# Optimization experiments

Measured on AMD Instinct MI355X. Metric: run time of the kernel, lower is better.

The kernel has to match this reference:

```python
import jax, jax.numpy as jnp
import numpy as np

N_NODES = 100000
N_EDGES = 1600000
NODE_DIM = 16
EDGE_DIM = 16
OUT_DIM = 16
H = 64  # edge/node/global hidden size
N_GRAPHS = 1


def _glorot(key, shape):
    fan_in, fan_out = shape[0], shape[1]
    lim = np.sqrt(6.0 / (fan_in + fan_out))
    return jax.random.uniform(key, shape, jnp.float32, -lim, lim)


def setup_inputs() -> dict:
    key = jax.random.key(0)
    ks = jax.random.split(key, 16)
    x = jax.random.normal(ks[0], (N_NODES, NODE_DIM), jnp.float32)
    edge_attr = jax.random.normal(ks[1], (N_EDGES, EDGE_DIM), jnp.float32)
    u = jax.random.normal(ks[2], (N_GRAPHS, H), jnp.float32)
    senders = jax.random.randint(ks[3], (N_EDGES,), 0, N_NODES, jnp.int32)
    receivers = jax.random.randint(ks[4], (N_EDGES,), 0, N_NODES, jnp.int32)
    node_gidx = jnp.zeros((N_NODES,), jnp.int32)
    edge_gidx = jnp.zeros((N_EDGES,), jnp.int32)
    # EdgeBlock MLP: in = edge + 2*node + global_h
    W_eb = _glorot(ks[5], (EDGE_DIM + 2 * NODE_DIM + H, H)); b_eb = jnp.zeros((H,), jnp.float32)
    # NodeBlock MLP: in = node + edge_h + global_h
    W_nb = _glorot(ks[6], (NODE_DIM + H + H, H)); b_nb = jnp.zeros((H,), jnp.float32)
    # GlobalBlock MLP: in = node_h + edge_h + global_h
    W_gb = _glorot(ks[7], (H + H + H, H)); b_gb = jnp.zeros((H,), jnp.float32)
    # node decoder: in = 2*edge_h + node_h + global_h -> H -> out
    W_d1 = _glorot(ks[8], (2 * H + H + H, H)); b_d1 = jnp.zeros((H,), jnp.float32)
    W_d2 = _glorot(ks[9], (H, OUT_DIM)); b_d2 = jnp.zeros((OUT_DIM,), jnp.float32)
    return dict(x=x, edge_attr=edge_attr, u=u, senders=senders, receivers=receivers,
                node_gidx=node_gidx, edge_gidx=edge_gidx,
                W_eb=W_eb, b_eb=b_eb, W_nb=W_nb, b_nb=b_nb, W_gb=W_gb, b_gb=b_gb,
                W_d1=W_d1, b_d1=b_d1, W_d2=W_d2, b_d2=b_d2)


def _segment_mean(data, ids, num_segments):
    s = jax.ops.segment_sum(data, ids, num_segments=num_segments)
    cnt = jax.ops.segment_sum(jnp.ones((data.shape[0], 1), data.dtype), ids, num_segments=num_segments)
    return s / jnp.maximum(cnt, 1.0)


def reference(x, edge_attr, u, senders, receivers, node_gidx, edge_gidx,
              W_eb, b_eb, W_nb, b_nb, W_gb, b_gb, W_d1, b_d1, W_d2, b_d2):
    # ---- GN1: EdgeBlock (gather -> concat -> linear+relu) ----
    e_in = jnp.concatenate([edge_attr, x[receivers], x[senders], u[edge_gidx]], axis=-1)  # [E, 112]
    e_h = jax.nn.relu(e_in @ W_eb + b_eb)  # [E, H]
    # ---- GN1: NodeBlock (scatter_add of received edges) ----
    agg_recv = jax.ops.segment_sum(e_h, receivers, num_segments=x.shape[0])  # [N, H]
    n_in = jnp.concatenate([agg_recv, x, u[node_gidx]], axis=-1)
    n_h = jax.nn.relu(n_in @ W_nb + b_nb)  # [N, H]
    # ---- GN1: GlobalBlock (scatter_mean reductions) ----
    e_mean = _segment_mean(e_h, edge_gidx, u.shape[0])  # [B, H]
    n_mean = _segment_mean(n_h, node_gidx, u.shape[0])  # [B, H]
    g_in = jnp.concatenate([e_mean, n_mean, u], axis=-1)
    u2 = jax.nn.relu(g_in @ W_gb + b_gb)  # [B, H]
    # ---- GN2: node decoder block (scatter_mean sent + received edges) ----
    agg_recv2 = _segment_mean(e_h, receivers, x.shape[0])
    agg_sent2 = _segment_mean(e_h, senders, x.shape[0])
    d_in = jnp.concatenate([agg_recv2, agg_sent2, n_h, u2[node_gidx]], axis=-1)  # [N, 256]
    out = jax.nn.relu(d_in @ W_d1 + b_d1) @ W_d2 + b_d2  # [N, out_dim]
    return out
```

## Files before the change

### kernel.cpp

```cpp
#include <hip/hip_runtime.h>


typedef unsigned int uint;
typedef unsigned short ushort;
typedef __attribute__((ext_vector_type(8))) short bf16x8;
typedef __attribute__((ext_vector_type(4))) float f32x4;

#define BW 128
#define BSHIFT 7
#define NBMAX 784
#define DC 4096
#define EMASK 0x1FFFFFu
#define OMASK 0x1FFFFu

#define LDF4(p) (*reinterpret_cast<const float4*>(p))

__device__ __forceinline__ ushort f2bf(float f) {
  uint u = __float_as_uint(f);
  u += 0x7FFFu + ((u >> 16) & 1u);
  return (ushort)(u >> 16);
}

__device__ __forceinline__ int aswz(int row, int kb) {
  return row * 64 + ((kb ^ (row & 7)) << 3);
}
__device__ __forceinline__ int nswz(int row, int kb) {
  return row * 128 + (((kb & 8) | ((kb ^ row) & 7)) << 3);
}
__device__ __forceinline__ int aswz192(int row, int kb) {
  return row * 192 + (((kb & 24) | ((kb ^ row) & 7)) << 3);
}

__global__ __launch_bounds__(256) void init_kernel(
    const float* __restrict__ x, ushort* __restrict__ xb, int n16, int nxb,
    const int* __restrict__ receivers, const int* __restrict__ senders,
    uint* __restrict__ bcnt_r, uint* __restrict__ bcnt_s, int E, int NB,
    const float* __restrict__ u, const float* __restrict__ W_eb,
    const float* __restrict__ b_eb, const float* __restrict__ W_nb,
    const float* __restrict__ b_nb, const float* __restrict__ W_d1,
    const float* __restrict__ W_d2, float* __restrict__ eb_init,
    float* __restrict__ nb_init, ushort* __restrict__ wt_lin,
    ushort* __restrict__ wnb_img, ushort* __restrict__ wtd1_img,
    ushort* __restrict__ w2_img) {
  if (blockIdx.x == 0) {
    int j = threadIdx.x;
    if (j >= 64) return;
    float ae = b_eb[j], an = b_nb[j];
    for (int k = 0; k < 64; ++k) {
      float uk = u[k];
      ae = fmaf(uk, W_eb[(48 + k) * 64 + j], ae);
      an = fmaf(uk, W_nb[(80 + k) * 64 + j], an);
    }
    eb_init[j] = ae;
    nb_init[j] = an;
    for (int k = 0; k < 64; ++k)
      wt_lin[j * 64 + k] = (k < 48) ? f2bf(W_eb[k * 64 + j]) : (ushort)0;
    for (int k = 0; k < 128; ++k) {
      ushort v = (k < 80) ? f2bf(W_nb[k * 64 + j]) : (ushort)0;
      wnb_img[nswz(j, k >> 3) + (k & 7)] = v;
    }
    for (int k = 0; k < 192; ++k)
      wtd1_img[aswz192(j, k >> 3) + (k & 7)] = f2bf(W_d1[k * 64 + j]);
    if (j < 16)
      for (int k = 0; k < 64; ++k)
        w2_img[aswz(j, k >> 3) + (k & 7)] = f2bf(W_d2[k * 16 + j]);
    return;
  }
  if (blockIdx.x <= nxb) {
    int i = (blockIdx.x - 1) * 256 + threadIdx.x;
    if (i * 4 >= n16) return;
    float4 a = LDF4(x + i * 4);
    ushort4 o = {f2bf(a.x), f2bf(a.y), f2bf(a.z), f2bf(a.w)};
    *reinterpret_cast<ushort4*>(xb + i * 4) = o;
    return;
  }
  __shared__ uint hr[NBMAX], hs[NBMAX];
  int t = threadIdx.x;
  int bid = blockIdx.x - 1 - nxb;
  for (int i = t; i < NB; i += 256) { hr[i] = 0; hs[i] = 0; }
  __syncthreads();
  int stride = 64 * 256;
  for (int e = bid * 256 + t; e < E; e += stride) {
    atomicAdd(&hr[receivers[e] >> BSHIFT], 1u);
    atomicAdd(&hs[senders[e] >> BSHIFT], 1u);
  }
  __syncthreads();
  for (int i = t; i < NB; i += 256) {
    if (hr[i]) atomicAdd(&bcnt_r[i], hr[i]);
    if (hs[i]) atomicAdd(&bcnt_s[i], hs[i]);
  }
}

__global__ __launch_bounds__(256) void bscan_kernel(
    const uint* __restrict__ bcnt_r, const uint* __restrict__ bcnt_s,
    uint* __restrict__ start_r, uint* __restrict__ start_s,
    uint* __restrict__ cur_r, uint* __restrict__ cur_s, int E, int NB) {
  __shared__ uint ts[256];
  int t = threadIdx.x;
  #pragma unroll
  for (int pass = 0; pass < 2; ++pass) {
    const uint* cnt = pass ? bcnt_s : bcnt_r;
    uint* start = pass ? start_s : start_r;
    uint* cur = pass ? cur_s : cur_r;
    uint loc[4]; uint tsum = 0;
    #pragma unroll
    for (int q = 0; q < 4; ++q) {
      int i = t * 4 + q;
      loc[q] = (i < NB) ? cnt[i] : 0;
      tsum += loc[q];
    }
    ts[t] = tsum;
    __syncthreads();
    for (int off = 1; off < 256; off <<= 1) {
      uint a = (t >= off) ? ts[t - off] : 0;
      __syncthreads();
      ts[t] += a;
      __syncthreads();
    }
    uint run = ts[t] - tsum;
    #pragma unroll
    for (int q = 0; q < 4; ++q) {
      int i = t * 4 + q;
      if (i < NB) { start[i] = run; cur[i] = run; run += loc[q]; }
    }
    if (t == 0) start[NB] = (uint)E;
    __syncthreads();
  }
}

__global__ __launch_bounds__(256) void distribute_kernel(
    const int* __restrict__ receivers, const int* __restrict__ senders,
    uint* __restrict__ gcur_r, uint* __restrict__ gcur_s,
    uint2* __restrict__ tmp_r, uint2* __restrict__ tmp_s, int E, int NB) {
  __shared__ uint hist[NBMAX], lstart[NBMAX], cur[NBMAX], gbase[NBMAX];
  __shared__ uint2 ids[DC];
  __shared__ ushort idsB[DC];
  __shared__ uint ts[256];
  int dir = blockIdx.x & 1;
  const int* key = dir ? senders : receivers;
  const int* oth = dir ? receivers : senders;
  uint* g_cursor = dir ? gcur_s : gcur_r;
  uint2* tmp = dir ? tmp_s : tmp_r;
  int t = threadIdx.x;
  int base = (blockIdx.x >> 1) * DC;
  int cact = min(DC, E - base);
  for (int i = t; i < NB; i += 256) hist[i] = 0;
  __syncthreads();
  for (int k = 0; k < DC / 256; ++k) {
    int j = k * 256 + t;
    if (j < cact) atomicAdd(&hist[key[base + j] >> BSHIFT], 1u);
  }
  __syncthreads();
  {
    uint loc[4]; uint tsum = 0;
    #pragma unroll
    for (int q = 0; q < 4; ++q) {
      int i = t * 4 + q;
      loc[q] = (i < NB) ? hist[i] : 0;
      tsum += loc[q];
    }
    ts[t] = tsum;
    __syncthreads();
    for (int off = 1; off < 256; off <<= 1) {
      uint a = (t >= off) ? ts[t - off] : 0;
      __syncthreads();
      ts[t] += a;
      __syncthreads();
    }
    uint run = ts[t] - tsum;
    #pragma unroll
    for (int q = 0; q < 4; ++q) {
      int i = t * 4 + q;
      if (i < NB) { lstart[i] = run; cur[i] = run; run += loc[q]; }
    }
  }
  __syncthreads();
  for (int i = t; i < NB; i += 256)
    if (hist[i]) gbase[i] = atomicAdd(&g_cursor[i], hist[i]);
  for (int k = 0; k < DC / 256; ++k) {
    int j = k * 256 + t;
    if (j < cact) {
      int e = base + j;
      int kk = key[e];
      uint b = (uint)(kk >> BSHIFT);
      uint slot = atomicAdd(&cur[b], 1u);
      ids[slot] = uint2{((uint)(kk & (BW - 1)) << 21) | (uint)e,
                        (uint)oth[e]};
      idsB[slot] = (ushort)b;
    }
  }
  __syncthreads();
  for (int j = t; j < cact; j += 256) {
    uint b2 = idsB[j];
    tmp[gbase[b2] + ((uint)j - lstart[b2])] = ids[j];
  }
}

__global__ __launch_bounds__(256) void bucketsort_kernel(
    const uint2* __restrict__ tmp_r, const uint2* __restrict__ tmp_s,
    const uint* __restrict__ start_r, const uint* __restrict__ start_s,
    uint2* __restrict__ srt_r, uint2* __restrict__ srt_s,
    uint* __restrict__ cnt_r, uint* __restrict__ cnt_s, int N) {
  __shared__ uint hist[BW], pfx[BW], cur[BW];
  int d = blockIdx.x & 1;
  int b = blockIdx.x >> 1;
  const uint2* tmp = d ? tmp_s : tmp_r;
  const uint* start = d ? start_s : start_r;
  uint2* srt = d ? srt_s : srt_r;
  uint* cnt = d ? cnt_s : cnt_r;
  int t = threadIdx.x;
  if (t < BW) hist[t] = 0;
  __syncthreads();
  int beg = (int)start[b], end = (int)start[b + 1];
  for (int i = beg + t; i < end; i += 256)
    atomicAdd(&hist[tmp[i].x >> 21], 1u);
  __syncthreads();
  if (t < BW) pfx[t] = hist[t];
  __syncthreads();
  for (int off = 1; off < BW; off <<= 1) {
    uint a = 0;
    if (t < BW && t >= off) a = pfx[t - off];
    __syncthreads();
    if (t < BW) pfx[t] += a;
    __syncthreads();
  }
  if (t < BW) cur[t] = pfx[t] - hist[t];
  __syncthreads();
  uint bhi = (uint)b << 17;
  for (int i = beg + t; i < end; i += 256) {
    uint2 v = tmp[i];
    uint nl = v.x >> 21;
    uint p = beg + atomicAdd(&cur[nl], 1u);
    srt[p] = uint2{v.x, bhi | v.y};
  }
  int nbase = b * BW;
  if (t < BW && nbase + t < N) cnt[nbase + t] = hist[t];
}

__global__ __launch_bounds__(256, 4) void escatter_kernel(
    const float* __restrict__ edge_attr, const ushort* __restrict__ xb,
    const uint2* __restrict__ srt_r, const uint2* __restrict__ srt_s,
    const ushort* __restrict__ wt_lin, const float* __restrict__ eb_init,
    float* __restrict__ sum_recv, float* __restrict__ sum_sent, int E,
    int ntiles) {
  __shared__ float Clds[4][16 * 72];
  __shared__ int nodeW[4][16];
  int t = threadIdx.x;
  int wid = t >> 6, l = t & 63;
  int lrow = l & 15, lk = l >> 4;
  bf16x8 b0[4], b1[4];
  float ebi[4];
  #pragma unroll
  for (int nt = 0; nt < 4; ++nt) {
    const ushort* wr = wt_lin + (nt * 16 + lrow) * 64;
    b0[nt] = *reinterpret_cast<const bf16x8*>(wr + lk * 8);
    b1[nt] = *reinterpret_cast<const bf16x8*>(wr + 32 + lk * 8);
    ebi[nt] = eb_init[nt * 16 + lrow];
  }
  const bf16x8 zero8 = {0, 0, 0, 0, 0, 0, 0, 0};
  int dir = blockIdx.x & 1;
  const uint2* srt = dir ? srt_s : srt_r;
  float* sum = dir ? sum_sent : sum_recv;
  int gw = (blockIdx.x >> 1) * 4 + wid;
  int nw = (gridDim.x >> 1) * 4;

  uint2 vC = {0, 0}, vN = {0, 0};
  bf16x8 a0C = zero8, a1C = zero8;

  if (gw < ntiles) {
    vC = srt[min(gw * 16 + lrow, E - 1)];
    int e = (int)(vC.x & EMASK);
    int kn = (int)((vC.y >> 17) * BW + (vC.x >> 21));
    int on = (int)(vC.y & OMASK);
    int s = dir ? kn : on;
    int r = dir ? on : kn;
    if (lk < 2) {
      const float* ap = edge_attr + (size_t)e * 16 + lk * 8;
      float4 f0 = LDF4(ap), f1 = LDF4(ap + 4);
      union { ushort h[8]; bf16x8 v; } pk;
      pk.h[0] = f2bf(f0.x); pk.h[1] = f2bf(f0.y);
      pk.h[2] = f2bf(f0.z); pk.h[3] = f2bf(f0.w);
      pk.h[4] = f2bf(f1.x); pk.h[5] = f2bf(f1.y);
      pk.h[6] = f2bf(f1.z); pk.h[7] = f2bf(f1.w);
      a0C = pk.v;
      a1C = *reinterpret_cast<const bf16x8*>(xb + (size_t)s * 16 + lk * 8);
    } else {
      a0C = *reinterpret_cast<const bf16x8*>(xb + (size_t)r * 16 +
                                             (lk - 2) * 8);
      a1C = zero8;
    }
  }
  if (gw + nw < ntiles) vN = srt[min((gw + nw) * 16 + lrow, E - 1)];

  for (int tile = gw; tile < ntiles; tile += nw) {
    bool hasN = (tile + nw) < ntiles;
    bool has2 = (tile + 2 * nw) < ntiles;
    bf16x8 a0N = zero8, a1N = zero8;
    if (hasN) {
      int e = (int)(vN.x & EMASK);
      int kn = (int)((vN.y >> 17) * BW + (vN.x >> 21));
      int on = (int)(vN.y & OMASK);
      int s = dir ? kn : on;
      int r = dir ? on : kn;
      if (lk < 2) {
        const float* ap = edge_attr + (size_t)e * 16 + lk * 8;
        float4 f0 = LDF4(ap), f1 = LDF4(ap + 4);
        union { ushort h[8]; bf16x8 v; } pk;
        pk.h[0] = f2bf(f0.x); pk.h[1] = f2bf(f0.y);
        pk.h[2] = f2bf(f0.z); pk.h[3] = f2bf(f0.w);
        pk.h[4] = f2bf(f1.x); pk.h[5] = f2bf(f1.y);
        pk.h[6] = f2bf(f1.z); pk.h[7] = f2bf(f1.w);
        a0N = pk.v;
        a1N = *reinterpret_cast<const bf16x8*>(xb + (size_t)s * 16 + lk * 8);
      } else {
        a0N = *reinterpret_cast<const bf16x8*>(xb + (size_t)r * 16 +
                                               (lk - 2) * 8);
      }
    }
    uint2 v2 = {0, 0};
    if (has2) v2 = srt[min((tile + 2 * nw) * 16 + lrow, E - 1)];
    if (lk == 0)
      nodeW[wid][lrow] = (int)((vC.y >> 17) * BW + (vC.x >> 21));
    f32x4 acc[4];
    #pragma unroll
    for (int nt = 0; nt < 4; ++nt) {
      acc[nt] = f32x4{ebi[nt], ebi[nt], ebi[nt], ebi[nt]};
      acc[nt] =
          __builtin_amdgcn_mfma_f32_16x16x32_bf16(a0C, b0[nt], acc[nt], 0, 0, 0);
      acc[nt] =
          __builtin_amdgcn_mfma_f32_16x16x32_bf16(a1C, b1[nt], acc[nt], 0, 0, 0);
    }
    int m0 = (l >> 4) * 4;
    #pragma unroll
    for (int nt = 0; nt < 4; ++nt) {
      #pragma unroll
      for (int reg = 0; reg < 4; ++reg) {
        Clds[wid][(m0 + reg) * 72 + nt * 16 + lrow] =
            fmaxf(acc[nt][reg], 0.f);
      }
    }
    int vc = min(16, E - tile * 16);
    float accum = 0.f;
    int prev = nodeW[wid][0];
    for (int mm = 0; mm < vc; ++mm) {
      int nd = nodeW[wid][mm];
      float v = Clds[wid][mm * 72 + l];
      if (nd != prev) {
        atomicAdd(&sum[(size_t)prev * 64 + l], accum);
        accum = 0.f;
        prev = nd;
      }
      accum += v;
    }
    atomicAdd(&sum[(size_t)prev * 64 + l], accum);
    vC = vN; a0C = a0N; a1C = a1N; vN = v2;
  }
}

__global__ __launch_bounds__(256, 2) void node_mfma_kernel(
    const float* __restrict__ sum_recv, const ushort* __restrict__ xb,
    const ushort* __restrict__ wnb_img, const float* __restrict__ nb_init,
    ushort* __restrict__ n_h, float* __restrict__ e_sum,
    float* __restrict__ n_sum, int N) {
  __shared__ ushort Alds[64 * 128];
  __shared__ ushort Wlds[64 * 128];
  __shared__ ushort Clds[4][16 * 72];
  int t = threadIdx.x;
  int base = blockIdx.x * 64;
  {
    const uint4* src = reinterpret_cast<const uint4*>(wnb_img);
    uint4* dst = reinterpret_cast<uint4*>(Wlds);
    #pragma unroll
    for (int i = 0; i < 4; ++i) dst[t + 256 * i] = src[t + 256 * i];
  }
  {
    int m = t >> 2, part = t & 3;
    int n = base + m;
    bool val = n < N;
    if (part < 2) {
      #pragma unroll
      for (int q = 0; q < 4; ++q) {
        int c = part * 4 + q;
        union { ushort h[8]; uint4 qq; } pk;
        if (val) {
          const float* src = sum_recv + (size_t)n * 64 + c * 8;
          float4 f0 = LDF4(src), f1 = LDF4(src + 4);
          pk.h[0] = f2bf(f0.x); pk.h[1] = f2bf(f0.y);
          pk.h[2] = f2bf(f0.z); pk.h[3] = f2bf(f0.w);
          pk.h[4] = f2bf(f1.x); pk.h[5] = f2bf(f1.y);
          pk.h[6] = f2bf(f1.z); pk.h[7] = f2bf(f1.w);
        } else {
          pk.qq = uint4{0, 0, 0, 0};
        }
        *reinterpret_cast<uint4*>(&Alds[nswz(m, c)]) = pk.qq;
      }
    } else if (part == 2) {
      uint4 w0 = {0, 0, 0, 0}, w1 = {0, 0, 0, 0};
      if (val) {
        const uint4* xp = reinterpret_cast<const uint4*>(xb + (size_t)n * 16);
        w0 = xp[0]; w1 = xp[1];
      }
      *reinterpret_cast<uint4*>(&Alds[nswz(m, 8)]) = w0;
      *reinterpret_cast<uint4*>(&Alds[nswz(m, 9)]) = w1;
      *reinterpret_cast<uint4*>(&Alds[nswz(m, 10)]) = uint4{0, 0, 0, 0};
      *reinterpret_cast<uint4*>(&Alds[nswz(m, 11)]) = uint4{0, 0, 0, 0};
    } else {
      #pragma unroll
      for (int q = 0; q < 4; ++q)
        *reinterpret_cast<uint4*>(&Alds[nswz(m, 12 + q)]) = uint4{0, 0, 0, 0};
    }
  }
  __syncthreads();
  int wid = t >> 6, l = t & 63;
  int lrow = l & 15, lk = l >> 4;
  int arow = wid * 16 + lrow;
  bf16x8 afr[4];
  #pragma unroll
  for (int g = 0; g < 4; ++g)
    afr[g] = *reinterpret_cast<const bf16x8*>(&Alds[nswz(arow, g * 4 + lk)]);
  f32x4 acc[4];
  #pragma unroll
  for (int nt = 0; nt < 4; ++nt) {
    float nbi = nb_init[nt * 16 + lrow];
    acc[nt] = f32x4{nbi, nbi, nbi, nbi};
    #pragma unroll
    for (int g = 0; g < 4; ++g) {
      bf16x8 b = *reinterpret_cast<const bf16x8*>(
          &Wlds[nswz(nt * 16 + lrow, g * 4 + lk)]);
      acc[nt] =
          __builtin_amdgcn_mfma_f32_16x16x32_bf16(afr[g], b, acc[nt], 0, 0, 0);
    }
  }
  int m0 = (l >> 4) * 4;
  #pragma unroll
  for (int nt = 0; nt < 4; ++nt) {
    #pragma unroll
    for (int reg = 0; reg < 4; ++reg) {
      Clds[wid][(m0 + reg) * 72 + nt * 16 + lrow] =
          f2bf(fmaxf(acc[nt][reg], 0.f));
    }
  }
  __syncthreads();
  int sm = l >> 2, ch = l & 3;
  int gn = base + wid * 16 + sm;
  uint4 c0 = *reinterpret_cast<const uint4*>(&Clds[wid][sm * 72 + ch * 16]);
  uint4 c1 = *reinterpret_cast<const uint4*>(&Clds[wid][sm * 72 + ch * 16 + 8]);
  if (gn < N) {
    uint4* dst = reinterpret_cast<uint4*>(n_h + (size_t)gn * 64 + ch * 16);
    dst[0] = c0;
    dst[1] = c1;
  }
  float* scr = reinterpret_cast<float*>(Alds);
  {
    int col = t & 63, rg = t >> 6;
    float pe = 0.f, pn = 0.f;
    #pragma unroll
    for (int rr = 0; rr < 16; ++rr) {
      int n = base + rg * 16 + rr;
      if (n < N) {
        pe += sum_recv[(size_t)n * 64 + col];
        pn += __uint_as_float((uint)Clds[rg][rr * 72 + col] << 16);
      }
    }
    scr[rg * 64 + col] = pe;
    scr[256 + rg * 64 + col] = pn;
  }
  __syncthreads();
  if (t < 64) {
    float se = scr[t] + scr[64 + t] + scr[128 + t] + scr[192 + t];
    float sn = scr[256 + t] + scr[320 + t] + scr[384 + t] + scr[448 + t];
    atomicAdd(&e_sum[t], se);
    atomicAdd(&n_sum[t], sn);
  }
}

__global__ __launch_bounds__(256, 2) void decoder_mfma_kernel(
    const float* __restrict__ sum_recv, const float* __restrict__ sum_sent,
    const uint* __restrict__ cnt_r, const uint* __restrict__ cnt_s,
    const ushort* __restrict__ n_h, const ushort* __restrict__ wtd1_img,
    const ushort* __restrict__ w2_img, const float* __restrict__ b_d2,
    const float* __restrict__ u, const float* __restrict__ e_sum,
    const float* __restrict__ n_sum, const float* __restrict__ W_gb,
    const float* __restrict__ b_gb, const float* __restrict__ W_d1,
    const float* __restrict__ b_d1, float* __restrict__ out, float invE,
    float invN, int N) {
  __shared__ ushort Alds[64 * 192];
  __shared__ ushort Wlds[64 * 192];
  __shared__ ushort Hlds[64 * 64];
  __shared__ ushort W2lds[16 * 64];
  __shared__ float gin[192], u2s[64], d1i[64];
  int t = threadIdx.x;
  int base = blockIdx.x * 64;
  {
    const uint4* src = reinterpret_cast<const uint4*>(wtd1_img);
    uint4* dst = reinterpret_cast<uint4*>(Wlds);
    #pragma unroll
    for (int i = 0; i < 6; ++i) dst[t + 256 * i] = src[t + 256 * i];
    if (t < 128)
      reinterpret_cast<uint4*>(W2lds)[t] =
          reinterpret_cast<const uint4*>(w2_img)[t];
  }
  {
    int m = t >> 2;
    int n = base + m;
    bool val = n < N;
    float invr = 0.f, invs = 0.f;
    if (val) {
      invr = 1.f / fmaxf((float)cnt_r[n], 1.f);
      invs = 1.f / fmaxf((float)cnt_s[n], 1.f);
    }
    int c0 = (t & 3) * 6;
    for (int c = c0; c < c0 + 6; ++c) {
      union { ushort h[8]; uint4 q; } pk;
      if (val) {
        if (c >= 16) {
          pk.q = *reinterpret_cast<const uint4*>(n_h + (size_t)n * 64 +
                                                 (c - 16) * 8);
        } else {
          const float* src;
          float scl;
          if (c < 8) { src = sum_recv + (size_t)n * 64 + c * 8; scl = invr; }
          else       { src = sum_sent + (size_t)n * 64 + (c - 8) * 8; scl = invs; }
          float4 f0 = LDF4(src), f1 = LDF4(src + 4);
          pk.h[0] = f2bf(f0.x * scl); pk.h[1] = f2bf(f0.y * scl);
          pk.h[2] = f2bf(f0.z * scl); pk.h[3] = f2bf(f0.w * scl);
          pk.h[4] = f2bf(f1.x * scl); pk.h[5] = f2bf(f1.y * scl);
          pk.h[6] = f2bf(f1.z * scl); pk.h[7] = f2bf(f1.w * scl);
        }
      } else {
        pk.q = uint4{0, 0, 0, 0};
      }
      *reinterpret_cast<uint4*>(&Alds[aswz192(m, c)]) = pk.q;
    }
  }
  if (t < 64) {
    gin[t] = e_sum[t] * invE;
    gin[64 + t] = n_sum[t] * invN;
    gin[128 + t] = u[t];
  }
  __syncthreads();
  if (t < 64) {
    float a = b_gb[t];
    for (int k = 0; k < 192; ++k) a = fmaf(gin[k], W_gb[k * 64 + t], a);
    u2s[t] = fmaxf(a, 0.f);
  }
  __syncthreads();
  if (t < 64) {
    float d = b_d1[t];
    for (int k = 0; k < 64; ++k) d = fmaf(u2s[k], W_d1[(192 + k) * 64 + t], d);
    d1i[t] = d;
  }
  __syncthreads();
  int wid = t >> 6, l = t & 63;
  int lrow = l & 15, lk = l >> 4;
  int arow = wid * 16 + lrow;
  bf16x8 afr[6];
  #pragma unroll
  for (int g = 0; g < 6; ++g)
    afr[g] = *reinterpret_cast<const bf16x8*>(&Alds[aswz192(arow, g * 4 + lk)]);
  f32x4 acc[4];
  #pragma unroll
  for (int nt = 0; nt < 4; ++nt) {
    float di = d1i[nt * 16 + lrow];
    acc[nt] = f32x4{di, di, di, di};
    #pragma unroll
    for (int g = 0; g < 6; ++g) {
      bf16x8 b = *reinterpret_cast<const bf16x8*>(
          &Wlds[aswz192(nt * 16 + lrow, g * 4 + lk)]);
      acc[nt] =
          __builtin_amdgcn_mfma_f32_16x16x32_bf16(afr[g], b, acc[nt], 0, 0, 0);
    }
  }
  int m0 = (l >> 4) * 4;
  #pragma unroll
  for (int nt = 0; nt < 4; ++nt) {
    #pragma unroll
    for (int reg = 0; reg < 4; ++reg) {
      int hm = wid * 16 + m0 + reg;
      int hn = nt * 16 + lrow;
      Hlds[hm * 64 + (((hn >> 3) ^ (hm & 7)) << 3) + (hn & 7)] =
          f2bf(fmaxf(acc[nt][reg], 0.f));
    }
  }
  __syncthreads();
  bf16x8 a20 = *reinterpret_cast<const bf16x8*>(&Hlds[aswz(arow, lk)]);
  bf16x8 a21 = *reinterpret_cast<const bf16x8*>(&Hlds[aswz(arow, 4 + lk)]);
  bf16x8 b20 = *reinterpret_cast<const bf16x8*>(&W2lds[aswz(lrow, lk)]);
  bf16x8 b21 = *reinterpret_cast<const bf16x8*>(&W2lds[aswz(lrow, 4 + lk)]);
  float bi = b_d2[lrow];
  f32x4 o = f32x4{bi, bi, bi, bi};
  o = __builtin_amdgcn_mfma_f32_16x16x32_bf16(a20, b20, o, 0, 0, 0);
  o = __builtin_amdgcn_mfma_f32_16x16x32_bf16(a21, b21, o, 0, 0, 0);
  #pragma unroll
  for (int reg = 0; reg < 4; ++reg) {
    int ge = base + wid * 16 + m0 + reg;
    if (ge < N) out[(size_t)ge * 16 + lrow] = o[reg];
  }
}

extern "C" void kernel_launch(void* const* d_in, const int* in_sizes, int n_in,
                              void* d_out, int out_size, void* d_ws,
                              size_t ws_size, hipStream_t stream) {
  const float* x         = (const float*)d_in[0];
  const float* edge_attr = (const float*)d_in[1];
  const float* u         = (const float*)d_in[2];
  const int*   senders   = (const int*)d_in[3];
  const int*   receivers = (const int*)d_in[4];
  const float* W_eb = (const float*)d_in[7];
  const float* b_eb = (const float*)d_in[8];
  const float* W_nb = (const float*)d_in[9];
  const float* b_nb = (const float*)d_in[10];
  const float* W_gb = (const float*)d_in[11];
  const float* b_gb = (const float*)d_in[12];
  const float* W_d1 = (const float*)d_in[13];
  const float* b_d1 = (const float*)d_in[14];
  const float* W_d2 = (const float*)d_in[15];
  const float* b_d2 = (const float*)d_in[16];

  int N = in_sizes[0] / 16;
  int E = in_sizes[1] / 16;
  int NB = (N + BW - 1) >> BSHIFT;
  int NDB = (E + DC - 1) / DC;
  int ntiles = (E + 15) / 16;
  int nxb = (N * 16 / 4 + 255) / 256;

  char* w = (char*)d_ws;
  float* sum_recv = (float*)w;       w += (size_t)N * 64 * 4;
  float* sum_sent = (float*)w;       w += (size_t)N * 64 * 4;
  ushort* n_h = (ushort*)w;          w += (size_t)N * 64 * 2;
  uint2* tmp_r = (uint2*)w;          w += (size_t)E * 8;
  uint2* tmp_s = (uint2*)w;          w += (size_t)E * 8;
  uint2* srt_r = (uint2*)w;          w += (size_t)E * 8;
  uint2* srt_s = (uint2*)w;          w += (size_t)E * 8;
  uint* cnt_r = (uint*)w;            w += (size_t)N * 4;
  uint* cnt_s = (uint*)w;            w += (size_t)N * 4;
  ushort* xb = (ushort*)w;           w += (size_t)N * 16 * 2;
  ushort* wt_lin = (ushort*)w;       w += (size_t)64 * 64 * 2;
  ushort* wnb_img = (ushort*)w;      w += (size_t)64 * 128 * 2;
  ushort* wtd1_img = (ushort*)w;     w += (size_t)64 * 192 * 2;
  ushort* w2_img = (ushort*)w;       w += (size_t)16 * 64 * 2;
  uint* start_r = (uint*)w;          w += (size_t)(NB + 1) * 4;
  uint* start_s = (uint*)w;          w += (size_t)(NB + 1) * 4;
  uint* cur_r = (uint*)w;            w += (size_t)NB * 4;
  uint* cur_s = (uint*)w;            w += (size_t)NB * 4;
  uint* bcnt_r = (uint*)w;           w += (size_t)NBMAX * 4;
  uint* bcnt_s = (uint*)w;           w += (size_t)NBMAX * 4;
  float* e_sum = (float*)w;          w += 64 * 4;
  float* n_sum = (float*)w;          w += 64 * 4;
  float* eb_init = (float*)w;        w += 64 * 4;
  float* nb_init = (float*)w;        w += 64 * 4;

  size_t zero_bytes = (size_t)(2 * NBMAX + 128) * 4;
  hipMemsetAsync(bcnt_r, 0, zero_bytes, stream);
  hipMemsetAsync(sum_recv, 0, (size_t)N * 128 * 4, stream);

  hipLaunchKernelGGL(init_kernel, dim3(1 + nxb + 64), dim3(256), 0, stream, x,
                     xb, N * 16, nxb, receivers, senders, bcnt_r, bcnt_s, E,
                     NB, u, W_eb, b_eb, W_nb, b_nb, W_d1, W_d2, eb_init,
                     nb_init, wt_lin, wnb_img, wtd1_img, w2_img);
  hipLaunchKernelGGL(bscan_kernel, dim3(1), dim3(256), 0, stream, bcnt_r,
                     bcnt_s, start_r, start_s, cur_r, cur_s, E, NB);
  hipLaunchKernelGGL(distribute_kernel, dim3(2 * NDB), dim3(256), 0, stream,
                     receivers, senders, cur_r, cur_s, tmp_r, tmp_s, E, NB);
  hipLaunchKernelGGL(bucketsort_kernel, dim3(2 * NB), dim3(256), 0, stream,
                     tmp_r, tmp_s, start_r, start_s, srt_r, srt_s, cnt_r,
                     cnt_s, N);
  hipLaunchKernelGGL(escatter_kernel, dim3(4096), dim3(256), 0, stream,
                     edge_attr, xb, srt_r, srt_s, wt_lin, eb_init, sum_recv,
                     sum_sent, E, ntiles);
  hipLaunchKernelGGL(node_mfma_kernel, dim3((N + 63) / 64), dim3(256), 0,
                     stream, sum_recv, xb, wnb_img, nb_init, n_h, e_sum,
                     n_sum, N);
  hipLaunchKernelGGL(decoder_mfma_kernel, dim3((N + 63) / 64), dim3(256), 0,
                     stream, sum_recv, sum_sent, cnt_r, cnt_s, n_h, wtd1_img,
                     w2_img, b_d2, u, e_sum, n_sum, W_gb, b_gb, W_d1, b_d1,
                     (float*)d_out, 1.0f / (float)E, 1.0f / (float)N, N);
}
```

Before: 396.2 us.

## Fuse per-bucket local sort into edge MLP scatter kernel

Removes the separate bucketsort kernel and its sorted global arrays. Each escatter block now takes one coarse bucket, stages its entries in LDS in chunks, builds a local node-ordered permutation, and runs the MFMA edge MLP and segmented atomic scatter directly from it. Per-node counts are accumulated atomically into a zeroed buffer. This saves one launch and a full read/write pass over the edge index arrays. In exchange, grid size is tied to the bucket count, it uses more LDS per block, and large buckets go through a serial chunk loop with extra barriers.

```diff
diff --git a/kernel.cpp b/kernel.cpp
--- a/kernel.cpp
+++ b/kernel.cpp
@@ -10,8 +10,8 @@
 #define BSHIFT 7
 #define NBMAX 784
 #define DC 4096
+#define CAP 1536
 #define EMASK 0x1FFFFFu
-#define OMASK 0x1FFFFu
 
 #define LDF4(p) (*reinterpret_cast<const float4*>(p))
 
@@ -196,53 +196,16 @@
   }
 }
 
-__global__ __launch_bounds__(256) void bucketsort_kernel(
+__global__ __launch_bounds__(256, 4) void escatter_kernel(
+    const float* __restrict__ edge_attr, const ushort* __restrict__ xb,
     const uint2* __restrict__ tmp_r, const uint2* __restrict__ tmp_s,
     const uint* __restrict__ start_r, const uint* __restrict__ start_s,
-    uint2* __restrict__ srt_r, uint2* __restrict__ srt_s,
-    uint* __restrict__ cnt_r, uint* __restrict__ cnt_s, int N) {
+    const ushort* __restrict__ wt_lin, const float* __restrict__ eb_init,
+    float* __restrict__ sum_recv, float* __restrict__ sum_sent,
+    uint* __restrict__ cnt_r, uint* __restrict__ cnt_s, int E, int N) {
+  __shared__ uint2 stage[CAP];
+  __shared__ ushort ord[CAP];
   __shared__ uint hist[BW], pfx[BW], cur[BW];
-  int d = blockIdx.x & 1;
-  int b = blockIdx.x >> 1;
-  const uint2* tmp = d ? tmp_s : tmp_r;
-  const uint* start = d ? start_s : start_r;
-  uint2* srt = d ? srt_s : srt_r;
-  uint* cnt = d ? cnt_s : cnt_r;
-  int t = threadIdx.x;
-  if (t < BW) hist[t] = 0;
-  __syncthreads();
-  int beg = (int)start[b], end = (int)start[b + 1];
-  for (int i = beg + t; i < end; i += 256)
-    atomicAdd(&hist[tmp[i].x >> 21], 1u);
-  __syncthreads();
-  if (t < BW) pfx[t] = hist[t];
-  __syncthreads();
-  for (int off = 1; off < BW; off <<= 1) {
-    uint a = 0;
-    if (t < BW && t >= off) a = pfx[t - off];
-    __syncthreads();
-    if (t < BW) pfx[t] += a;
-    __syncthreads();
-  }
-  if (t < BW) cur[t] = pfx[t] - hist[t];
-  __syncthreads();
-  uint bhi = (uint)b << 17;
-  for (int i = beg + t; i < end; i += 256) {
-    uint2 v = tmp[i];
-    uint nl = v.x >> 21;
-    uint p = beg + atomicAdd(&cur[nl], 1u);
-    srt[p] = uint2{v.x, bhi | v.y};
-  }
-  int nbase = b * BW;
-  if (t < BW && nbase + t < N) cnt[nbase + t] = hist[t];
-}
-
-__global__ __launch_bounds__(256, 4) void escatter_kernel(
-    const float* __restrict__ edge_attr, const ushort* __restrict__ xb,
-    const uint2* __restrict__ srt_r, const uint2* __restrict__ srt_s,
-    const ushort* __restrict__ wt_lin, const float* __restrict__ eb_init,
-    float* __restrict__ sum_recv, float* __restrict__ sum_sent, int E,
-    int ntiles) {
   __shared__ float Clds[4][16 * 72];
   __shared__ int nodeW[4][16];
   int t = threadIdx.x;
@@ -259,47 +222,51 @@
   }
   const bf16x8 zero8 = {0, 0, 0, 0, 0, 0, 0, 0};
   int dir = blockIdx.x & 1;
-  const uint2* srt = dir ? srt_s : srt_r;
+  int b = blockIdx.x >> 1;
+  const uint2* tmp = dir ? tmp_s : tmp_r;
+  const uint* start = dir ? start_s : start_r;
   float* sum = dir ? sum_sent : sum_recv;
-  int gw = (blockIdx.x >> 1) * 4 + wid;
-  int nw = (gridDim.x >> 1) * 4;
-
-  uint2 vC = {0, 0}, vN = {0, 0};
-  bf16x8 a0C = zero8, a1C = zero8;
-
-  if (gw < ntiles) {
-    vC = srt[min(gw * 16 + lrow, E - 1)];
-    int e = (int)(vC.x & EMASK);
-    int kn = (int)((vC.y >> 17) * BW + (vC.x >> 21));
-    int on = (int)(vC.y & OMASK);
-    int s = dir ? kn : on;
-    int r = dir ? on : kn;
-    if (lk < 2) {
-      const float* ap = edge_attr + (size_t)e * 16 + lk * 8;
-      float4 f0 = LDF4(ap), f1 = LDF4(ap + 4);
-      union { ushort h[8]; bf16x8 v; } pk;
-      pk.h[0] = f2bf(f0.x); pk.h[1] = f2bf(f0.y);
-      pk.h[2] = f2bf(f0.z); pk.h[3] = f2bf(f0.w);
-      pk.h[4] = f2bf(f1.x); pk.h[5] = f2bf(f1.y);
-      pk.h[6] = f2bf(f1.z); pk.h[7] = f2bf(f1.w);
-      a0C = pk.v;
-      a1C = *reinterpret_cast<const bf16x8*>(xb + (size_t)s * 16 + lk * 8);
-    } else {
-      a0C = *reinterpret_cast<const bf16x8*>(xb + (size_t)r * 16 +
-                                             (lk - 2) * 8);
-      a1C = zero8;
-    }
-  }
-  if (gw + nw < ntiles) vN = srt[min((gw + nw) * 16 + lrow, E - 1)];
-
-  for (int tile = gw; tile < ntiles; tile += nw) {
-    bool hasN = (tile + nw) < ntiles;
-    bool has2 = (tile + 2 * nw) < ntiles;
-    bf16x8 a0N = zero8, a1N = zero8;
-    if (hasN) {
-      int e = (int)(vN.x & EMASK);
-      int kn = (int)((vN.y >> 17) * BW + (vN.x >> 21));
-      int on = (int)(vN.y & OMASK);
+  uint* cnt = dir ? cnt_s : cnt_r;
+  int beg = (int)start[b], end = (int)start[b + 1];
+  int nbase = b * BW;
+
+  for (int cbeg = beg; cbeg < end; cbeg += CAP) {
+    int cc = min(CAP, end - cbeg);
+    if (t < BW) hist[t] = 0;
+    __syncthreads();
+    for (int i = t; i < cc; i += 256) {
+      uint2 v = tmp[cbeg + i];
+      stage[i] = v;
+      atomicAdd(&hist[v.x >> 21], 1u);
+    }
+    __syncthreads();
+    if (t < BW && hist[t] && nbase + t < N) atomicAdd(&cnt[nbase + t], hist[t]);
+    if (t < BW) pfx[t] = hist[t];
+    __syncthreads();
+    for (int off = 1; off < BW; off <<= 1) {
+      uint a = 0;
+      if (t < BW && t >= off) a = pfx[t - off];
+      __syncthreads();
+      if (t < BW) pfx[t] += a;
+      __syncthreads();
+    }
+    if (t < BW) cur[t] = pfx[t] - hist[t];
+    __syncthreads();
+    for (int i = t; i < cc; i += 256) {
+      uint nl = stage[i].x >> 21;
+      uint p = atomicAdd(&cur[nl], 1u);
+      ord[p] = (ushort)i;
+    }
+    __syncthreads();
+    int ntile = (cc + 15) >> 4;
+    uint2 vC = {0, 0}, vN = {0, 0};
+    bf16x8 a0C = zero8, a1C = zero8;
+    if (wid < ntile) {
+      int j = min(wid * 16 + lrow, cc - 1);
+      vC = stage[ord[j]];
+      int e = (int)(vC.x & EMASK);
+      int kn = nbase + (int)(vC.x >> 21);
+      int on = (int)vC.y;
       int s = dir ? kn : on;
       int r = dir ? on : kn;
       if (lk < 2) {
@@ -310,50 +277,75 @@
         pk.h[2] = f2bf(f0.z); pk.h[3] = f2bf(f0.w);
         pk.h[4] = f2bf(f1.x); pk.h[5] = f2bf(f1.y);
         pk.h[6] = f2bf(f1.z); pk.h[7] = f2bf(f1.w);
-        a0N = pk.v;
-        a1N = *reinterpret_cast<const bf16x8*>(xb + (size_t)s * 16 + lk * 8);
+        a0C = pk.v;
+        a1C = *reinterpret_cast<const bf16x8*>(xb + (size_t)s * 16 + lk * 8);
       } else {
-        a0N = *reinterpret_cast<const bf16x8*>(xb + (size_t)r * 16 +
+        a0C = *reinterpret_cast<const bf16x8*>(xb + (size_t)r * 16 +
                                                (lk - 2) * 8);
       }
     }
-    uint2 v2 = {0, 0};
-    if (has2) v2 = srt[min((tile + 2 * nw) * 16 + lrow, E - 1)];
-    if (lk == 0)
-      nodeW[wid][lrow] = (int)((vC.y >> 17) * BW + (vC.x >> 21));
-    f32x4 acc[4];
-    #pragma unroll
-    for (int nt = 0; nt < 4; ++nt) {
-      acc[nt] = f32x4{ebi[nt], ebi[nt], ebi[nt], ebi[nt]};
-      acc[nt] =
-          __builtin_amdgcn_mfma_f32_16x16x32_bf16(a0C, b0[nt], acc[nt], 0, 0, 0);
-      acc[nt] =
-          __builtin_amdgcn_mfma_f32_16x16x32_bf16(a1C, b1[nt], acc[nt], 0, 0, 0);
-    }
-    int m0 = (l >> 4) * 4;
-    #pragma unroll
-    for (int nt = 0; nt < 4; ++nt) {
+    for (int wt = wid; wt < ntile; wt += 4) {
+      int wtN = wt + 4;
+      bf16x8 a0N = zero8, a1N = zero8;
+      if (wtN < ntile) {
+        int j = min(wtN * 16 + lrow, cc - 1);
+        vN = stage[ord[j]];
+        int e = (int)(vN.x & EMASK);
+        int kn = nbase + (int)(vN.x >> 21);
+        int on = (int)vN.y;
+        int s = dir ? kn : on;
+        int r = dir ? on : kn;
+        if (lk < 2) {
+          const float* ap = edge_attr + (size_t)e * 16 + lk * 8;
+          float4 f0 = LDF4(ap), f1 = LDF4(ap + 4);
+          union { ushort h[8]; bf16x8 v; } pk;
+          pk.h[0] = f2bf(f0.x); pk.h[1] = f2bf(f0.y);
+          pk.h[2] = f2bf(f0.z); pk.h[3] = f2bf(f0.w);
+          pk.h[4] = f2bf(f1.x); pk.h[5] = f2bf(f1.y);
+          pk.h[6] = f2bf(f1.z); pk.h[7] = f2bf(f1.w);
+          a0N = pk.v;
+          a1N = *reinterpret_cast<const bf16x8*>(xb + (size_t)s * 16 + lk * 8);
+        } else {
+          a0N = *reinterpret_cast<const bf16x8*>(xb + (size_t)r * 16 +
+                                                 (lk - 2) * 8);
+        }
+      }
+      if (lk == 0) nodeW[wid][lrow] = nbase + (int)(vC.x >> 21);
+      f32x4 acc[4];
       #pragma unroll
-      for (int reg = 0; reg < 4; ++reg) {
-        Clds[wid][(m0 + reg) * 72 + nt * 16 + lrow] =
-            fmaxf(acc[nt][reg], 0.f);
-      }
-    }
-    int vc = min(16, E - tile * 16);
-    float accum = 0.f;
-    int prev = nodeW[wid][0];
-    for (int mm = 0; mm < vc; ++mm) {
-      int nd = nodeW[wid][mm];
-      float v = Clds[wid][mm * 72 + l];
-      if (nd != prev) {
-        atomicAdd(&sum[(size_t)prev * 64 + l], accum);
-        accum = 0.f;
-        prev = nd;
-      }
-      accum += v;
-    }
-    atomicAdd(&sum[(size_t)prev * 64 + l], accum);
-    vC = vN; a0C = a0N; a1C = a1N; vN = v2;
+      for (int nt = 0; nt < 4; ++nt) {
+        acc[nt] = f32x4{ebi[nt], ebi[nt], ebi[nt], ebi[nt]};
+        acc[nt] = __builtin_amdgcn_mfma_f32_16x16x32_bf16(a0C, b0[nt], acc[nt],
+                                                          0, 0, 0);
+        acc[nt] = __builtin_amdgcn_mfma_f32_16x16x32_bf16(a1C, b1[nt], acc[nt],
+                                                          0, 0, 0);
+      }
+      int m0 = (l >> 4) * 4;
+      #pragma unroll
+      for (int nt = 0; nt < 4; ++nt) {
+        #pragma unroll
+        for (int reg = 0; reg < 4; ++reg) {
+          Clds[wid][(m0 + reg) * 72 + nt * 16 + lrow] =
+              fmaxf(acc[nt][reg], 0.f);
+        }
+      }
+      int vc = min(16, cc - wt * 16);
+      float accum = 0.f;
+      int prev = nodeW[wid][0];
+      for (int mm = 0; mm < vc; ++mm) {
+        int nd = nodeW[wid][mm];
+        float v = Clds[wid][mm * 72 + l];
+        if (nd != prev) {
+          atomicAdd(&sum[(size_t)prev * 64 + l], accum);
+          accum = 0.f;
+          prev = nd;
+        }
+        accum += v;
+      }
+      atomicAdd(&sum[(size_t)prev * 64 + l], accum);
+      vC = vN; a0C = a0N; a1C = a1N;
+    }
+    __syncthreads();
   }
 }
 
@@ -621,7 +613,6 @@
   int E = in_sizes[1] / 16;
   int NB = (N + BW - 1) >> BSHIFT;
   int NDB = (E + DC - 1) / DC;
-  int ntiles = (E + 15) / 16;
   int nxb = (N * 16 / 4 + 255) / 256;
 
   char* w = (char*)d_ws;
@@ -630,10 +621,6 @@
   ushort* n_h = (ushort*)w;          w += (size_t)N * 64 * 2;
   uint2* tmp_r = (uint2*)w;          w += (size_t)E * 8;
   uint2* tmp_s = (uint2*)w;          w += (size_t)E * 8;
-  uint2* srt_r = (uint2*)w;          w += (size_t)E * 8;
-  uint2* srt_s = (uint2*)w;          w += (size_t)E * 8;
-  uint* cnt_r = (uint*)w;            w += (size_t)N * 4;
-  uint* cnt_s = (uint*)w;            w += (size_t)N * 4;
   ushort* xb = (ushort*)w;           w += (size_t)N * 16 * 2;
   ushort* wt_lin = (ushort*)w;       w += (size_t)64 * 64 * 2;
   ushort* wnb_img = (ushort*)w;      w += (size_t)64 * 128 * 2;
@@ -643,6 +630,8 @@
   uint* start_s = (uint*)w;          w += (size_t)(NB + 1) * 4;
   uint* cur_r = (uint*)w;            w += (size_t)NB * 4;
   uint* cur_s = (uint*)w;            w += (size_t)NB * 4;
+  uint* cnt_r = (uint*)w;            w += (size_t)N * 4;
+  uint* cnt_s = (uint*)w;            w += (size_t)N * 4;
   uint* bcnt_r = (uint*)w;           w += (size_t)NBMAX * 4;
   uint* bcnt_s = (uint*)w;           w += (size_t)NBMAX * 4;
   float* e_sum = (float*)w;          w += 64 * 4;
@@ -650,8 +639,8 @@
   float* eb_init = (float*)w;        w += 64 * 4;
   float* nb_init = (float*)w;        w += 64 * 4;
 
-  size_t zero_bytes = (size_t)(2 * NBMAX + 128) * 4;
-  hipMemsetAsync(bcnt_r, 0, zero_bytes, stream);
+  size_t zero_bytes = ((size_t)2 * N + 2 * NBMAX + 128) * 4;
+  hipMemsetAsync(cnt_r, 0, zero_bytes, stream);
   hipMemsetAsync(sum_recv, 0, (size_t)N * 128 * 4, stream);
 
   hipLaunchKernelGGL(init_kernel, dim3(1 + nxb + 64), dim3(256), 0, stream, x,
@@ -662,12 +651,9 @@
                      bcnt_s, start_r, start_s, cur_r, cur_s, E, NB);
   hipLaunchKernelGGL(distribute_kernel, dim3(2 * NDB), dim3(256), 0, stream,
                      receivers, senders, cur_r, cur_s, tmp_r, tmp_s, E, NB);
-  hipLaunchKernelGGL(bucketsort_kernel, dim3(2 * NB), dim3(256), 0, stream,
-                     tmp_r, tmp_s, start_r, start_s, srt_r, srt_s, cnt_r,
-                     cnt_s, N);
-  hipLaunchKernelGGL(escatter_kernel, dim3(4096), dim3(256), 0, stream,
-                     edge_attr, xb, srt_r, srt_s, wt_lin, eb_init, sum_recv,
-                     sum_sent, E, ntiles);
+  hipLaunchKernelGGL(escatter_kernel, dim3(2 * NB), dim3(256), 0, stream,
+                     edge_attr, xb, tmp_r, tmp_s, start_r, start_s, wt_lin,
+                     eb_init, sum_recv, sum_sent, cnt_r, cnt_s, E, N);
   hipLaunchKernelGGL(node_mfma_kernel, dim3((N + 63) / 64), dim3(256), 0,
                      stream, sum_recv, xb, wnb_img, nb_init, n_h, e_sum,
                      n_sum, N);
```

Measured after the change: 414.4 us. 4.6% more time.
